# Performance work log

Hardware: AMD Instinct MI355X
Metric: run time of the kernel (lower is better)

## Reference

```python
import jax, jax.numpy as jnp
import numpy as np

N_EMBD = 384
HEAD_SIZE = 64
B, T = 16, 2048


def setup_inputs() -> dict:
    key = jax.random.key(0)
    ks = jax.random.split(key, 7)
    s = 1.0 / np.sqrt(N_EMBD)
    return {
        "x": jax.random.normal(ks[0], (B, T, N_EMBD), dtype=jnp.float32),
        "Wq": jax.random.uniform(ks[1], (N_EMBD, HEAD_SIZE), jnp.float32, -s, s),
        "bq": jax.random.uniform(ks[2], (HEAD_SIZE,), jnp.float32, -s, s),
        "Wk": jax.random.uniform(ks[3], (N_EMBD, HEAD_SIZE), jnp.float32, -s, s),
        "bk": jax.random.uniform(ks[4], (HEAD_SIZE,), jnp.float32, -s, s),
        "Wv": jax.random.uniform(ks[5], (N_EMBD, HEAD_SIZE), jnp.float32, -s, s),
        "bv": jax.random.uniform(ks[6], (HEAD_SIZE,), jnp.float32, -s, s),
    }


def reference(x, Wq, bq, Wk, bk, Wv, bv):
    # QKV projections: [B,T,C] @ [C,H] -> [B,T,H]
    q = x @ Wq + bq
    k = x @ Wk + bk
    v = x @ Wv + bv
    scale = k.shape[-1] ** (-0.5)
    # NOTE: original forward applies NO causal mask (tril buffer unused).
    scores = jnp.einsum("bqh,bkh->bqk", q, k) * scale  # [B,T,T]
    wmap = jax.nn.softmax(scores, axis=-1)
    # dropout is identity in eval mode
    out = jnp.einsum("bqk,bkh->bqh", wmap, v)  # [B,T,H]
    return out
```

## Files before the change

kernel.cpp:

```cpp
#include <hip/hip_runtime.h>
#include <hip/hip_bf16.h>
#include <cstdint>

typedef unsigned short u16;
typedef __attribute__((ext_vector_type(8))) short short8;
typedef __attribute__((ext_vector_type(4))) short short4v;
typedef __attribute__((ext_vector_type(4))) float f32x4;

#define MFMA16(a, b, c) __builtin_amdgcn_mfma_f32_16x16x32_bf16((a), (b), (c), 0, 0, 0)

constexpr int Bn   = 16;
constexpr int Tn   = 2048;
constexpr int Cn   = 384;
constexpr int Hn   = 64;
constexpr long NTOK = (long)Bn * Tn;
constexpr long NELT = NTOK * Hn;
constexpr int SPLITS = 3;

#define QSCALE 0.18033688011112042f

__device__ __forceinline__ u16 f2bf(float f) {
  union { float f; uint32_t u; } c; c.f = f;
  uint32_t u = c.u;
  return (u16)((u + 0x7fffu + ((u >> 16) & 1u)) >> 16);
}

__device__ __forceinline__ uint32_t pkbf(float a, float b) {
  uint32_t d;
  asm("v_cvt_pk_bf16_f32 %0, %1, %2" : "=v"(d) : "v"(a), "v"(b));
  return d;
}

__device__ __forceinline__ short8 ldx8(const float* p) {
  const float4 f0 = *reinterpret_cast<const float4*>(p);
  const float4 f1 = *reinterpret_cast<const float4*>(p + 4);
  union { short8 s8; uint32_t u[4]; } r;
  r.u[0] = pkbf(f0.x, f0.y); r.u[1] = pkbf(f0.z, f0.w);
  r.u[2] = pkbf(f1.x, f1.y); r.u[3] = pkbf(f1.z, f1.w);
  return r.s8;
}

__device__ __forceinline__ void gl16(const u16* g, const u16* l) {
  __builtin_amdgcn_global_load_lds(
      (const __attribute__((address_space(1))) void*)g,
      (__attribute__((address_space(3))) void*)l, 16, 0, 0);
}

__global__ __launch_bounds__(256) void wtrans(
    const float* __restrict__ Wq, const float* __restrict__ Wk,
    const float* __restrict__ Wv, u16* __restrict__ wtd)
{
  __shared__ u16 tile[64][65];
  const int m  = blockIdx.x / 6;
  const int kc = blockIdx.x % 6;
  const float* W = (m == 0) ? Wq : (m == 1) ? Wk : Wv;
  const int t = threadIdx.x;

  {
    const int kr = t >> 2, seg = t & 3;
    const float* src = W + (size_t)(kc * 64 + kr) * Hn + seg * 16;
    #pragma unroll
    for (int j = 0; j < 4; ++j) {
      const float4 f = *reinterpret_cast<const float4*>(src + j * 4);
      u16* p = &tile[kr][seg * 16 + j * 4];
      p[0] = f2bf(f.x); p[1] = f2bf(f.y); p[2] = f2bf(f.z); p[3] = f2bf(f.w);
    }
  }
  __syncthreads();
  {
    const int hr = t >> 2, seg = t & 3;
    union { short8 s; u16 u[8]; } o0, o1;
    #pragma unroll
    for (int j = 0; j < 8; ++j) o0.u[j] = tile[seg * 16 + j][hr];
    #pragma unroll
    for (int j = 0; j < 8; ++j) o1.u[j] = tile[seg * 16 + 8 + j][hr];
    u16* dst = wtd + ((size_t)m * 64 + hr) * Cn + kc * 64 + seg * 16;
    *reinterpret_cast<short8*>(dst)     = o0.s;
    *reinterpret_cast<short8*>(dst + 8) = o1.s;
  }
}

__global__ __launch_bounds__(256, 2) void qkv_proj(
    const float* __restrict__ x, const u16* __restrict__ wtd,
    const float* __restrict__ bq, const float* __restrict__ bk,
    const float* __restrict__ bv,
    u16* __restrict__ oq, u16* __restrict__ ok, u16* __restrict__ ovt)
{
  __shared__ u16 wbuf[3][3 * 64 * 64];

  const int t    = threadIdx.x;
  const int lane = t & 63;
  const int w    = t >> 6;
  const int l15  = lane & 15;
  const int lh   = lane >> 4;
  const long r0  = (long)blockIdx.x * 64;

  int srcoff[6];
  #pragma unroll
  for (int i = 0; i < 6; ++i) {
    const int g = i * 256 + t;
    const int r = g >> 3, c = g & 7;
    srcoff[i] = r * Cn + ((c ^ (r & 7)) << 3);
  }
  const int ldsb = w * 64 * 8;

  const float* xrow = x + (r0 + w * 16 + l15) * Cn;

  const int cks0 = ((lh)     ^ (l15 & 7)) << 3;
  const int cks1 = ((lh + 4) ^ (l15 & 7)) << 3;

  f32x4 acc[3][4];
  #pragma unroll
  for (int m = 0; m < 3; ++m)
    #pragma unroll
    for (int n = 0; n < 4; ++n) acc[m][n] = f32x4{0.f, 0.f, 0.f, 0.f};

  #pragma unroll
  for (int i = 0; i < 6; ++i)
    gl16(wtd + srcoff[i], &wbuf[0][(i * 256) * 8 + ldsb]);
  short8 aCur0 = ldx8(xrow + lh * 8);
  short8 aCur1 = ldx8(xrow + 32 + lh * 8);
  #pragma unroll
  for (int i = 0; i < 6; ++i)
    gl16(wtd + 64 + srcoff[i], &wbuf[1][(i * 256) * 8 + ldsb]);
  short8 aNx10 = ldx8(xrow + 64 + lh * 8);
  short8 aNx11 = ldx8(xrow + 96 + lh * 8);
  short8 aNx20, aNx21;
  asm volatile("s_waitcnt vmcnt(14)" ::: "memory");
  __builtin_amdgcn_s_barrier();
  __builtin_amdgcn_sched_barrier(0);

  for (int kc = 0; kc < 6; ++kc) {
    const int cb = kc % 3;
    const int sb = (kc + 2) % 3;
    if (kc + 2 < 6) {
      #pragma unroll
      for (int i = 0; i < 6; ++i)
        gl16(wtd + (kc + 2) * 64 + srcoff[i], &wbuf[sb][(i * 256) * 8 + ldsb]);
      const float* p = xrow + (kc + 2) * 64 + lh * 8;
      aNx20 = ldx8(p);
      aNx21 = ldx8(p + 32);
    }

    const u16* wc = &wbuf[cb][0];
    #pragma unroll
    for (int m = 0; m < 3; ++m)
      #pragma unroll
      for (int n = 0; n < 4; ++n) {
        const int row = m * 64 + n * 16 + l15;
        const short8 b0 = *reinterpret_cast<const short8*>(&wc[row * 64 + cks0]);
        acc[m][n] = MFMA16(aCur0, b0, acc[m][n]);
        const short8 b1 = *reinterpret_cast<const short8*>(&wc[row * 64 + cks1]);
        acc[m][n] = MFMA16(aCur1, b1, acc[m][n]);
      }

    if (kc + 1 < 6) {
      if (kc + 2 < 6) asm volatile("s_waitcnt vmcnt(14)" ::: "memory");
      else            asm volatile("s_waitcnt vmcnt(4)"  ::: "memory");
      __builtin_amdgcn_s_barrier();
      __builtin_amdgcn_sched_barrier(0);
      aCur0 = aNx10; aCur1 = aNx11;
      aNx10 = aNx20; aNx11 = aNx21;
    }
  }

  {
    const float* bias[2] = {bq, bk};
    u16*         dst[2]  = {oq, ok};
    const float  scl[2]  = {QSCALE, 1.0f};
    #pragma unroll
    for (int m = 0; m < 2; ++m) {
      #pragma unroll
      for (int n = 0; n < 4; ++n) {
        int col = n * 16 + l15;
        float bb = bias[m][col];
        #pragma unroll
        for (int r = 0; r < 4; ++r) {
          int row = lh * 4 + r;
          dst[m][(r0 + w * 16 + row) * Hn + col] = f2bf((acc[m][n][r] + bb) * scl[m]);
        }
      }
    }
  }
  {
    const long g    = r0 + w * 16 + lh * 4;
    const long bidx = g >> 11;
    const long tloc = g & 2047;
    const int  u    = (int)(tloc & 63);
    const long tb   = tloc & ~63L;
    const int  slotb = 32 * ((u >> 5) & 1) + 8 * ((u >> 2) & 3) + 4 * ((u >> 4) & 1);
    #pragma unroll
    for (int n = 0; n < 4; ++n) {
      int col = n * 16 + l15;
      float bb = bv[col];
      short4v pk;
      #pragma unroll
      for (int r = 0; r < 4; ++r) pk[r] = (short)f2bf(acc[2][n][r] + bb);
      *reinterpret_cast<short4v*>(ovt + (bidx * Hn + col) * Tn + tb + slotb) = pk;
    }
  }
}

__global__ __launch_bounds__(256, 3) void flash_attn(
    const u16* __restrict__ q, const u16* __restrict__ k,
    const u16* __restrict__ vt, float* __restrict__ opart,
    float* __restrict__ lpart)
{
  __shared__ u16 kbuf[3][64 * 64];
  __shared__ u16 vbuf[3][64 * 64];

  const int t    = threadIdx.x;
  const int lane = t & 63;
  const int w    = t >> 6;
  const int l15  = lane & 15;
  const int lh   = lane >> 4;
  const int swz_id = (blockIdx.x & 7) * 96 + (blockIdx.x >> 3);
  const int b     = swz_id / 48;
  const int rsw   = swz_id % 48;
  const int split = rsw / 16;
  const int qt    = rsw % 16;
  const long rowbase = (long)b * Tn + qt * 128;
  const int it0 = (split * 32) / 3;
  const int it1 = ((split + 1) * 32) / 3;

  short8 aq[2][2];
  #pragma unroll
  for (int qg = 0; qg < 2; ++qg) {
    const u16* qrow = q + (rowbase + w * 32 + qg * 16 + l15) * Hn;
    aq[qg][0] = *reinterpret_cast<const short8*>(qrow + lh * 8);
    aq[qg][1] = *reinterpret_cast<const short8*>(qrow + 32 + lh * 8);
  }

  f32x4 o[2][4];
  #pragma unroll
  for (int qg = 0; qg < 2; ++qg)
    #pragma unroll
    for (int m = 0; m < 4; ++m) o[qg][m] = f32x4{0.f, 0.f, 0.f, 0.f};
  float lacc[2] = {0.f, 0.f};

  const u16* kb_g = k  + (long)b * Tn * Hn;
  const u16* vb_g = vt + (long)b * Hn * Tn;

  const int g0 = t, g1 = 256 + t;
  const int r0g = g0 >> 3, c0g = g0 & 7;
  const int r1g = g1 >> 3, c1g = g1 & 7;
  const long ksrc0 = (long)r0g * Hn + ((c0g ^ (r0g & 7)) << 3);
  const long ksrc1 = (long)r1g * Hn + ((c1g ^ (r1g & 7)) << 3);
  const long vsrc0 = (long)r0g * Tn + ((c0g ^ (r0g & 7)) << 3);
  const long vsrc1 = (long)r1g * Tn + ((c1g ^ (r1g & 7)) << 3);
  const int wb0 = w * 64 * 8;
  const int wb1 = wb0 + 256 * 8;

  const int swz  = l15 & 7;
  const int cks0 = ((0 * 4 + lh) ^ swz) << 3;
  const int cks1 = ((1 * 4 + lh) ^ swz) << 3;
  const int rfr  = l15 * 64;

  {
    const u16* kt = kb_g + (long)it0 * 64 * Hn;
    const u16* vp = vb_g + it0 * 64;
    gl16(kt + ksrc0, &kbuf[0][wb0]);
    gl16(kt + ksrc1, &kbuf[0][wb1]);
    gl16(vp + vsrc0, &vbuf[0][wb0]);
    gl16(vp + vsrc1, &vbuf[0][wb1]);
    const u16* kt1 = kb_g + (long)(it0 + 1) * 64 * Hn;
    const u16* vp1 = vb_g + (it0 + 1) * 64;
    gl16(kt1 + ksrc0, &kbuf[1][wb0]);
    gl16(kt1 + ksrc1, &kbuf[1][wb1]);
    gl16(vp1 + vsrc0, &vbuf[1][wb0]);
    gl16(vp1 + vsrc1, &vbuf[1][wb1]);
  }
  asm volatile("s_waitcnt vmcnt(4)" ::: "memory");
  __builtin_amdgcn_s_barrier();
  __builtin_amdgcn_sched_barrier(0);

  for (int it = it0; it < it1; ++it) {
    const int cb = (it - it0) % 3;
    const int sb = (it - it0 + 2) % 3;
    if (it + 2 < it1) {
      const u16* kt = kb_g + (long)(it + 2) * 64 * Hn;
      const u16* vp = vb_g + (it + 2) * 64;
      gl16(kt + ksrc0, &kbuf[sb][wb0]);
      gl16(kt + ksrc1, &kbuf[sb][wb1]);
      gl16(vp + vsrc0, &vbuf[sb][wb0]);
      gl16(vp + vsrc1, &vbuf[sb][wb1]);
    }

    const u16* kc  = &kbuf[cb][0];
    const u16* vcb = &vbuf[cb][0];

    f32x4 s0[4], s1[4];
    #pragma unroll
    for (int n = 0; n < 4; ++n) { s0[n] = f32x4{0.f,0.f,0.f,0.f}; s1[n] = f32x4{0.f,0.f,0.f,0.f}; }
    #pragma unroll
    for (int n = 0; n < 4; ++n) {
      const short8 ak0 = *reinterpret_cast<const short8*>(&kc[n * 1024 + rfr + cks0]);
      const short8 ak1 = *reinterpret_cast<const short8*>(&kc[n * 1024 + rfr + cks1]);
      s0[n] = MFMA16(ak0, aq[0][0], s0[n]);
      s0[n] = MFMA16(ak1, aq[0][1], s0[n]);
      s1[n] = MFMA16(ak0, aq[1][0], s1[n]);
      s1[n] = MFMA16(ak1, aq[1][1], s1[n]);
    }

    #pragma unroll
    for (int n = 0; n < 4; ++n)
      #pragma unroll
      for (int r = 0; r < 4; ++r) {
        s0[n][r] = __builtin_amdgcn_exp2f(s0[n][r]);
        s1[n][r] = __builtin_amdgcn_exp2f(s1[n][r]);
      }

    {
      float a0 = (s0[0][0]+s0[0][1])+(s0[0][2]+s0[0][3]);
      float a1 = (s0[1][0]+s0[1][1])+(s0[1][2]+s0[1][3]);
      float a2 = (s0[2][0]+s0[2][1])+(s0[2][2]+s0[2][3]);
      float a3 = (s0[3][0]+s0[3][1])+(s0[3][2]+s0[3][3]);
      lacc[0] += (a0 + a1) + (a2 + a3);
      float b0 = (s1[0][0]+s1[0][1])+(s1[0][2]+s1[0][3]);
      float b1 = (s1[1][0]+s1[1][1])+(s1[1][2]+s1[1][3]);
      float b2 = (s1[2][0]+s1[2][1])+(s1[2][2]+s1[2][3]);
      float b3 = (s1[3][0]+s1[3][1])+(s1[3][2]+s1[3][3]);
      lacc[1] += (b0 + b1) + (b2 + b3);
    }

    union { short8 s8; uint32_t u[4]; } B00, B01, B10, B11;
    B00.u[0] = pkbf(s0[0][0], s0[0][1]); B00.u[1] = pkbf(s0[0][2], s0[0][3]);
    B00.u[2] = pkbf(s0[1][0], s0[1][1]); B00.u[3] = pkbf(s0[1][2], s0[1][3]);
    B01.u[0] = pkbf(s0[2][0], s0[2][1]); B01.u[1] = pkbf(s0[2][2], s0[2][3]);
    B01.u[2] = pkbf(s0[3][0], s0[3][1]); B01.u[3] = pkbf(s0[3][2], s0[3][3]);
    B10.u[0] = pkbf(s1[0][0], s1[0][1]); B10.u[1] = pkbf(s1[0][2], s1[0][3]);
    B10.u[2] = pkbf(s1[1][0], s1[1][1]); B10.u[3] = pkbf(s1[1][2], s1[1][3]);
    B11.u[0] = pkbf(s1[2][0], s1[2][1]); B11.u[1] = pkbf(s1[2][2], s1[2][3]);
    B11.u[2] = pkbf(s1[3][0], s1[3][1]); B11.u[3] = pkbf(s1[3][2], s1[3][3]);

    #pragma unroll
    for (int m = 0; m < 4; ++m) {
      const short8 av0 = *reinterpret_cast<const short8*>(&vcb[m * 1024 + rfr + cks0]);
      const short8 av1 = *reinterpret_cast<const short8*>(&vcb[m * 1024 + rfr + cks1]);
      o[0][m] = MFMA16(av0, B00.s8, o[0][m]);
      o[0][m] = MFMA16(av1, B01.s8, o[0][m]);
      o[1][m] = MFMA16(av0, B10.s8, o[1][m]);
      o[1][m] = MFMA16(av1, B11.s8, o[1][m]);
    }

    if (it + 1 < it1) {
      if (it + 2 < it1) asm volatile("s_waitcnt vmcnt(4)" ::: "memory");
      else              asm volatile("s_waitcnt vmcnt(0)" ::: "memory");
      __builtin_amdgcn_s_barrier();
      __builtin_amdgcn_sched_barrier(0);
    }
  }

  #pragma unroll
  for (int qg = 0; qg < 2; ++qg) {
    float tot = lacc[qg];
    tot += __shfl_xor(tot, 16);
    tot += __shfl_xor(tot, 32);
    const long qrow = rowbase + w * 32 + qg * 16 + l15;
    float* od = opart + ((long)split * NELT) + qrow * Hn;
    #pragma unroll
    for (int m = 0; m < 4; ++m) {
      float4 vv;
      vv.x = o[qg][m][0]; vv.y = o[qg][m][1]; vv.z = o[qg][m][2]; vv.w = o[qg][m][3];
      *reinterpret_cast<float4*>(od + m * 16 + lh * 4) = vv;
    }
    if (lh == 0) lpart[(long)split * NTOK + qrow] = tot;
  }
}

__global__ __launch_bounds__(256) void combine(
    const float* __restrict__ op, const float* __restrict__ lp,
    float* __restrict__ out)
{
  const long idx  = (long)blockIdx.x * 256 + threadIdx.x;
  const long base = idx * 4;
  const long row  = base >> 6;
  float4 acc = *reinterpret_cast<const float4*>(op + base);
  float lsum = lp[row];
  #pragma unroll
  for (int s = 1; s < SPLITS; ++s) {
    const float4 c = *reinterpret_cast<const float4*>(op + s * NELT + base);
    acc.x += c.x; acc.y += c.y; acc.z += c.z; acc.w += c.w;
    lsum += lp[s * NTOK + row];
  }
  const float linv = 1.0f / lsum;
  float4 r;
  r.x = acc.x * linv; r.y = acc.y * linv; r.z = acc.z * linv; r.w = acc.w * linv;
  *reinterpret_cast<float4*>(out + base) = r;
}

extern "C" void kernel_launch(void* const* d_in, const int* in_sizes, int n_in,
                              void* d_out, int out_size, void* d_ws, size_t ws_size,
                              hipStream_t stream) {
  const float* x  = (const float*)d_in[0];
  const float* Wq = (const float*)d_in[1];
  const float* bq = (const float*)d_in[2];
  const float* Wk = (const float*)d_in[3];
  const float* bk = (const float*)d_in[4];
  const float* Wv = (const float*)d_in[5];
  const float* bv = (const float*)d_in[6];
  float* out = (float*)d_out;

  u16* qs  = (u16*)d_ws;
  u16* ks  = qs + NELT;
  u16* vs  = ks + NELT;
  u16* wtd = vs + NELT;
  float* op = (float*)(wtd + 3 * 64 * Cn);
  float* lp = op + (long)SPLITS * NELT;

  hipLaunchKernelGGL(wtrans, dim3(18), dim3(256), 0, stream, Wq, Wk, Wv, wtd);
  hipLaunchKernelGGL(qkv_proj, dim3((int)(NTOK / 64)), dim3(256), 0, stream,
                     x, wtd, bq, bk, bv, qs, ks, vs);
  hipLaunchKernelGGL(flash_attn, dim3(16 * 16 * SPLITS), dim3(256), 0, stream,
                     qs, ks, vs, op, lp);
  hipLaunchKernelGGL(combine, dim3((int)(NELT / 4 / 256)), dim3(256), 0, stream,
                     op, lp, out);
}
```

Before: 54.82 us.

## Retile QKV projection to 32-row blocks with 2x2 wave split and 32-wide K chunks

```diff
diff --git a/kernel.cpp b/kernel.cpp
--- a/kernel.cpp
+++ b/kernel.cpp
@@ -80,87 +80,81 @@
   }
 }
 
-__global__ __launch_bounds__(256, 2) void qkv_proj(
+__global__ __launch_bounds__(256, 4) void qkv_proj(
     const float* __restrict__ x, const u16* __restrict__ wtd,
     const float* __restrict__ bq, const float* __restrict__ bk,
     const float* __restrict__ bv,
     u16* __restrict__ oq, u16* __restrict__ ok, u16* __restrict__ ovt)
 {
-  __shared__ u16 wbuf[3][3 * 64 * 64];
+  __shared__ u16 wbuf[3][192 * 32];
 
   const int t    = threadIdx.x;
   const int lane = t & 63;
   const int w    = t >> 6;
+  const int wr   = w & 1;
+  const int wc   = w >> 1;
   const int l15  = lane & 15;
   const int lh   = lane >> 4;
-  const long r0  = (long)blockIdx.x * 64;
-
-  int srcoff[6];
-  #pragma unroll
-  for (int i = 0; i < 6; ++i) {
-    const int g = i * 256 + t;
-    const int r = g >> 3, c = g & 7;
-    srcoff[i] = r * Cn + ((c ^ (r & 7)) << 3);
-  }
-  const int ldsb = w * 64 * 8;
-
-  const float* xrow = x + (r0 + w * 16 + l15) * Cn;
-
-  const int cks0 = ((lh)     ^ (l15 & 7)) << 3;
-  const int cks1 = ((lh + 4) ^ (l15 & 7)) << 3;
-
-  f32x4 acc[3][4];
+  const long r0  = (long)blockIdx.x * 32;
+
+  int srcoff[3];
+  #pragma unroll
+  for (int i = 0; i < 3; ++i) {
+    const int gid = i * 256 + t;
+    const int r = gid >> 2, c = gid & 3;
+    srcoff[i] = r * Cn + ((c ^ ((r >> 1) & 3)) << 3);
+  }
+
+  const float* xrow = x + (r0 + wr * 16 + l15) * Cn;
+
+  const int cksw = (lh ^ ((l15 >> 1) & 3)) << 3;
+
+  f32x4 acc[3][2];
   #pragma unroll
   for (int m = 0; m < 3; ++m)
     #pragma unroll
-    for (int n = 0; n < 4; ++n) acc[m][n] = f32x4{0.f, 0.f, 0.f, 0.f};
-
-  #pragma unroll
-  for (int i = 0; i < 6; ++i)
-    gl16(wtd + srcoff[i], &wbuf[0][(i * 256) * 8 + ldsb]);
-  short8 aCur0 = ldx8(xrow + lh * 8);
-  short8 aCur1 = ldx8(xrow + 32 + lh * 8);
-  #pragma unroll
-  for (int i = 0; i < 6; ++i)
-    gl16(wtd + 64 + srcoff[i], &wbuf[1][(i * 256) * 8 + ldsb]);
-  short8 aNx10 = ldx8(xrow + 64 + lh * 8);
-  short8 aNx11 = ldx8(xrow + 96 + lh * 8);
-  short8 aNx20, aNx21;
-  asm volatile("s_waitcnt vmcnt(14)" ::: "memory");
+    for (int n = 0; n < 2; ++n) acc[m][n] = f32x4{0.f, 0.f, 0.f, 0.f};
+
+  #pragma unroll
+  for (int i = 0; i < 3; ++i)
+    gl16(wtd + srcoff[i], &wbuf[0][(i * 256 + w * 64) * 8]);
+  short8 aCur = ldx8(xrow + lh * 8);
+  #pragma unroll
+  for (int i = 0; i < 3; ++i)
+    gl16(wtd + 32 + srcoff[i], &wbuf[1][(i * 256 + w * 64) * 8]);
+  short8 aNx1 = ldx8(xrow + 32 + lh * 8);
+  short8 aNx2;
+  asm volatile("s_waitcnt vmcnt(7)" ::: "memory");
   __builtin_amdgcn_s_barrier();
   __builtin_amdgcn_sched_barrier(0);
 
-  for (int kc = 0; kc < 6; ++kc) {
+  for (int kc = 0; kc < 12; ++kc) {
     const int cb = kc % 3;
     const int sb = (kc + 2) % 3;
-    if (kc + 2 < 6) {
+    if (kc + 2 < 12) {
       #pragma unroll
-      for (int i = 0; i < 6; ++i)
-        gl16(wtd + (kc + 2) * 64 + srcoff[i], &wbuf[sb][(i * 256) * 8 + ldsb]);
-      const float* p = xrow + (kc + 2) * 64 + lh * 8;
-      aNx20 = ldx8(p);
-      aNx21 = ldx8(p + 32);
-    }
-
-    const u16* wc = &wbuf[cb][0];
+      for (int i = 0; i < 3; ++i)
+        gl16(wtd + (kc + 2) * 32 + srcoff[i], &wbuf[sb][(i * 256 + w * 64) * 8]);
+      aNx2 = ldx8(xrow + (kc + 2) * 32 + lh * 8);
+    }
+
+    const u16* wcb = &wbuf[cb][0];
     #pragma unroll
     for (int m = 0; m < 3; ++m)
       #pragma unroll
-      for (int n = 0; n < 4; ++n) {
-        const int row = m * 64 + n * 16 + l15;
-        const short8 b0 = *reinterpret_cast<const short8*>(&wc[row * 64 + cks0]);
-        acc[m][n] = MFMA16(aCur0, b0, acc[m][n]);
-        const short8 b1 = *reinterpret_cast<const short8*>(&wc[row * 64 + cks1]);
-        acc[m][n] = MFMA16(aCur1, b1, acc[m][n]);
+      for (int n = 0; n < 2; ++n) {
+        const int R = m * 64 + wc * 32 + n * 16 + l15;
+        const short8 bfr = *reinterpret_cast<const short8*>(&wcb[R * 32 + cksw]);
+        acc[m][n] = MFMA16(aCur, bfr, acc[m][n]);
       }
 
-    if (kc + 1 < 6) {
-      if (kc + 2 < 6) asm volatile("s_waitcnt vmcnt(14)" ::: "memory");
-      else            asm volatile("s_waitcnt vmcnt(4)"  ::: "memory");
+    if (kc + 1 < 12) {
+      if (kc + 2 < 12) asm volatile("s_waitcnt vmcnt(7)" ::: "memory");
+      else             asm volatile("s_waitcnt vmcnt(2)" ::: "memory");
       __builtin_amdgcn_s_barrier();
       __builtin_amdgcn_sched_barrier(0);
-      aCur0 = aNx10; aCur1 = aNx11;
-      aNx10 = aNx20; aNx11 = aNx21;
+      aCur = aNx1;
+      aNx1 = aNx2;
     }
   }
 
@@ -171,27 +165,27 @@
     #pragma unroll
     for (int m = 0; m < 2; ++m) {
       #pragma unroll
-      for (int n = 0; n < 4; ++n) {
-        int col = n * 16 + l15;
+      for (int n = 0; n < 2; ++n) {
+        int col = wc * 32 + n * 16 + l15;
         float bb = bias[m][col];
         #pragma unroll
         for (int r = 0; r < 4; ++r) {
           int row = lh * 4 + r;
-          dst[m][(r0 + w * 16 + row) * Hn + col] = f2bf((acc[m][n][r] + bb) * scl[m]);
+          dst[m][(r0 + wr * 16 + row) * Hn + col] = f2bf((acc[m][n][r] + bb) * scl[m]);
         }
       }
     }
   }
   {
-    const long g    = r0 + w * 16 + lh * 4;
+    const long g    = r0 + wr * 16 + lh * 4;
     const long bidx = g >> 11;
     const long tloc = g & 2047;
     const int  u    = (int)(tloc & 63);
     const long tb   = tloc & ~63L;
     const int  slotb = 32 * ((u >> 5) & 1) + 8 * ((u >> 2) & 3) + 4 * ((u >> 4) & 1);
     #pragma unroll
-    for (int n = 0; n < 4; ++n) {
-      int col = n * 16 + l15;
+    for (int n = 0; n < 2; ++n) {
+      int col = wc * 32 + n * 16 + l15;
       float bb = bv[col];
       short4v pk;
       #pragma unroll
@@ -409,7 +403,7 @@
   float* lp = op + (long)SPLITS * NELT;
 
   hipLaunchKernelGGL(wtrans, dim3(18), dim3(256), 0, stream, Wq, Wk, Wv, wtd);
-  hipLaunchKernelGGL(qkv_proj, dim3((int)(NTOK / 64)), dim3(256), 0, stream,
+  hipLaunchKernelGGL(qkv_proj, dim3((int)(NTOK / 32)), dim3(256), 0, stream,
                      x, wtd, bq, bk, bv, qs, ks, vs);
   hipLaunchKernelGGL(flash_attn, dim3(16 * 16 * SPLITS), dim3(256), 0, stream,
                      qs, ks, vs, op, lp);
```

Measured after the change: 63.13 us. 1.15x slower.
